# Optimization experiments

Hardware: AMD Instinct MI355X
Metric: run time of the kernel (lower is better)

## Reference

```python
import jax, jax.numpy as jnp
import numpy as np

B, P, N = 32, 128, 1000
EMB, H, QKV, FFH = 128, 8, 16, 128
LS = [11, 21]  # local_size + 1 per policy
PEN = -100000.0
CLIP = 10.0
EPS = 1e-5


def _policy_params(key, ls):
    ks = jax.random.split(key, 8)
    s = 0.05
    return dict(
        w1=jax.random.normal(ks[0], (2 * ls + 2, FFH)) * s, b1=jnp.zeros((FFH,)),
        w2=jax.random.normal(ks[1], (FFH, 2 * FFH)) * s, b2=jnp.zeros((2 * FFH,)),
        w3=jax.random.normal(ks[2], (2 * FFH, FFH)) * s, b3=jnp.zeros((FFH,)),
        w4=jax.random.normal(ks[3], (FFH, ls)) * 0.01, b4=jnp.zeros((ls,)),
        gamma=jnp.ones((2 * FFH,)), beta=jnp.zeros((2 * FFH,)),
    )


def setup_inputs() -> dict:
    key = jax.random.key(0)
    ks = jax.random.split(key, 16)
    s = 0.05
    d = {
        "encoded_last_node": jax.random.normal(ks[0], (B, P, EMB)),
        "load": jax.random.uniform(ks[1], (B, P)),
        "cur_dist": jax.random.uniform(ks[2], (B, P, N)),
        "cur_theta": jax.random.normal(ks[3], (B, P, N)),
        "ins_feat0": jax.random.normal(ks[4], (B, P, 1)),
        "ins_feat1": jax.random.normal(ks[5], (B, P, 1)),
        "ninf_mask": jnp.zeros((B, P, N)),
        "encoded_nodes": jax.random.normal(ks[6], (B, N, EMB)),
        "Wq_last": jax.random.normal(ks[7], (EMB + 1, H * QKV)) * s,
        "Wk": jax.random.normal(ks[8], (EMB, H * QKV)) * s,
        "Wv": jax.random.normal(ks[9], (EMB, H * QKV)) * s,
        "Wcomb": jax.random.normal(ks[10], (H * QKV, EMB)) * s,
        "bcomb": jnp.zeros((EMB,)),
    }
    for i, ls in enumerate(LS):
        pp = _policy_params(ks[11 + i], ls)
        for name, val in pp.items():
            d[f"p{i}_{name}"] = val
    return d


def _local_policy(theta, dist, f0, f1, w1, b1, w2, b2, w3, b3, w4, b4, gamma, beta, ls):
    # topk smallest distances
    neg_v, idx = jax.lax.top_k(-dist, ls)          # [B,P,ls]
    sd = -neg_v
    sd = sd / sd.max(-1, keepdims=True)
    st = jnp.take_along_axis(theta, idx, axis=-1)
    x = jnp.concatenate([sd, st, f0, f1], axis=-1)  # [B,P,2*ls+2]
    e = jax.nn.relu(x @ w1 + b1)
    h = jax.nn.relu(e @ w2 + b2)                    # [B,P,2*FFH]
    # InstanceNorm1d over the P (length) axis, per (batch, channel)
    mu = h.mean(axis=1, keepdims=True)
    var = h.var(axis=1, keepdims=True)
    h = (h - mu) * jax.lax.rsqrt(var + EPS) * gamma + beta
    e = jax.nn.relu(h @ w3 + b3)
    out = e @ w4 + b4 - sd                          # [B,P,ls]
    bi = jnp.arange(dist.shape[0])[:, None, None]
    pi = jnp.arange(dist.shape[1])[None, :, None]
    return jnp.full(dist.shape, PEN, dist.dtype).at[bi, pi, idx].set(out)


def reference(encoded_last_node, load, cur_dist, cur_theta, ins_feat0, ins_feat1,
              ninf_mask, encoded_nodes,
              Wq_last, Wk, Wv, Wcomb, bcomb,
              p0_w1, p0_b1, p0_w2, p0_b2, p0_w3, p0_b3, p0_w4, p0_b4, p0_gamma, p0_beta,
              p1_w1, p1_b1, p1_w2, p1_b2, p1_w3, p1_b3, p1_w4, p1_b4, p1_gamma, p1_beta):
    def rh(x):  # reshape_by_heads -> [B, H, n, QKV]
        b, n, _ = x.shape
        return x.reshape(b, n, H, QKV).transpose(0, 2, 1, 3)

    k = rh(encoded_nodes @ Wk)
    v = rh(encoded_nodes @ Wv)
    q = rh(jnp.concatenate([encoded_last_node, load[:, :, None]], axis=-1) @ Wq_last)

    score = jnp.einsum('bhpd,bhnd->bhpn', q, k) / jnp.sqrt(jnp.float32(QKV))
    score = score + ninf_mask[:, None, :, :]
    w = jax.nn.softmax(score, axis=-1)
    oc = jnp.einsum('bhpn,bhnd->bhpd', w, v).transpose(0, 2, 1, 3).reshape(B, P, H * QKV)
    mh = oc @ Wcomb + bcomb                                    # [B,P,EMB]

    sc = jnp.einsum('bpe,bne->bpn', mh, encoded_nodes) / jnp.sqrt(jnp.float32(EMB))

    sl0 = _local_policy(cur_theta, cur_dist, ins_feat0, ins_feat1,
                        p0_w1, p0_b1, p0_w2, p0_b2, p0_w3, p0_b3, p0_w4, p0_b4,
                        p0_gamma, p0_beta, LS[0])
    sl1 = _local_policy(cur_theta, cur_dist, ins_feat0, ins_feat1,
                        p1_w1, p1_b1, p1_w2, p1_b2, p1_w3, p1_b3, p1_w4, p1_b4,
                        p1_gamma, p1_beta, LS[1])
    sc = sc + (sl0 + sl1) / 2.0

    probs = jax.nn.softmax(CLIP * jnp.tanh(sc) + ninf_mask, axis=-1)
    return probs
```

## Files before the change

### kernel.cpp

```cpp
#include <hip/hip_runtime.h>
#include <math.h>

#define BB 32
#define PP 128
#define NN 1000
#define EMB 128
#define HH 8
#define FFH 128
#define PEN -100000.0f
#define CLIP 10.0f
#define EPS 1e-5f

__global__ __launch_bounds__(512) void mega1(
    const float* __restrict__ enc, const float* __restrict__ Wk, const float* __restrict__ Wv,
    float* __restrict__ Kb, float* __restrict__ Vb,
    const float* __restrict__ eln, const float* __restrict__ load,
    const float* __restrict__ Wq, float* __restrict__ Q,
    const float* __restrict__ mask, float* __restrict__ maskT,
    const float* __restrict__ dist, const float* __restrict__ theta,
    const float* __restrict__ f0, const float* __restrict__ f1,
    float* __restrict__ XS0, float* __restrict__ XS1,
    float* __restrict__ SD0, float* __restrict__ SD1, int* __restrict__ IDX) {
    __shared__ float smem[2112];
    int blk = blockIdx.x;
    int tid = threadIdx.x;
    if (blk < 512) {
        int half = blk & 1, chunk = (blk >> 1) & 7, b = blk >> 4;
        const float* W = half ? Wv : Wk;
        float* Ob = half ? Vb : Kb;
        int n0 = chunk * 125;
        float* A_s = smem;
        float* B_s = smem + 1056;
        int tr = tid >> 5, tc = tid & 31;
        float acc[8][4];
#pragma unroll
        for (int i = 0; i < 8; i++)
#pragma unroll
            for (int j = 0; j < 4; j++) acc[i][j] = 0.f;
        for (int kk = 0; kk < 128; kk += 8) {
#pragma unroll
            for (int f = tid; f < 1024; f += 512) {
                int node = f >> 3, k = f & 7;
                A_s[k * 132 + node] = (node < 125)
                    ? enc[((size_t)(b * 1000) + n0 + node) * 128 + kk + k] : 0.f;
            }
#pragma unroll
            for (int f = tid; f < 1024; f += 512) {
                int k = f >> 7, c = f & 127;
                B_s[k * 132 + c] = W[(kk + k) * 128 + c];
            }
            __syncthreads();
#pragma unroll
            for (int k = 0; k < 8; ++k) {
                float av[8], bv[4];
                *(float4*)&av[0] = *(const float4*)&A_s[k * 132 + tr * 8];
                *(float4*)&av[4] = *(const float4*)&A_s[k * 132 + tr * 8 + 4];
                *(float4*)&bv[0] = *(const float4*)&B_s[k * 132 + tc * 4];
#pragma unroll
                for (int i = 0; i < 8; ++i)
#pragma unroll
                    for (int j = 0; j < 4; ++j) acc[i][j] = fmaf(av[i], bv[j], acc[i][j]);
            }
            __syncthreads();
        }
#pragma unroll
        for (int i = 0; i < 8; ++i) {
            int node = tr * 8 + i;
            if (node < 125) {
                float4 o = {acc[i][0], acc[i][1], acc[i][2], acc[i][3]};
                *(float4*)(Ob + ((size_t)(b * 1000) + n0 + node) * 128 + tc * 4) = o;
            }
        }
    } else if (blk < 1024) {
        int r0 = (blk - 512) * 8;
        float* x_s = smem;
#pragma unroll
        for (int f = tid; f < 1024; f += 512) {
            int r = f >> 7, c = f & 127;
            x_s[r * 129 + c] = eln[(size_t)(r0 + r) * 128 + c];
        }
        if (tid < 8) x_s[tid * 129 + 128] = load[r0 + tid];
        __syncthreads();
        int rr = tid >> 7, c = tid & 127;
        float a0 = 0.f, a1 = 0.f;
#pragma unroll 4
        for (int k = 0; k < 128; ++k) {
            float wv = Wq[k * 128 + c];
            a0 = fmaf(x_s[rr * 129 + k], wv, a0);
            a1 = fmaf(x_s[(rr + 4) * 129 + k], wv, a1);
        }
        {
            float wv = Wq[16384 + c];
            a0 = fmaf(x_s[rr * 129 + 128], wv, a0);
            a1 = fmaf(x_s[(rr + 4) * 129 + 128], wv, a1);
        }
        Q[(size_t)(r0 + rr) * 128 + c] = a0 * 0.25f;
        Q[(size_t)(r0 + rr + 4) * 128 + c] = a1 * 0.25f;
    } else if (blk < 3072) {
        int t2 = (blk - 1024) * 2 + (tid >> 8);
        int tl = tid & 255;
        int b = t2 >> 7, pt = (t2 >> 5) & 3, nt = t2 & 31;
        int tx = tl & 31, ty = tl >> 5;
        float* t = smem + (tid >> 8) * 1056;
        int p0 = pt * 32, n0 = nt * 32;
#pragma unroll
        for (int r = 0; r < 32; r += 8) {
            int pp = p0 + ty + r, nn = n0 + tx;
            t[(ty + r) * 33 + tx] = (nn < 1000) ? mask[((size_t)b * 128 + pp) * 1000 + nn] : 0.f;
        }
        __syncthreads();
#pragma unroll
        for (int r = 0; r < 32; r += 8) {
            int nn = n0 + ty + r, pp = p0 + tx;
            if (nn < 1000) maskT[((size_t)b * 1000 + nn) * 128 + pp] = t[tx * 33 + ty + r];
        }
    } else {
        int w = tid >> 6, lane = tid & 63;
        int bp = (blk - 3072) * 8 + w;
        const float* drow = dist + (size_t)bp * 1000;
        unsigned long long key[16];
#pragma unroll
        for (int j = 0; j < 16; ++j) {
            int n = j * 64 + lane;
            key[j] = (n < 1000)
                ? ((((unsigned long long)__float_as_uint(drow[n])) << 32) | (unsigned)n)
                : ~0ull;
        }
        float myv = 0.f, v10 = 0.f, v20 = 0.f;
        int myi = 0;
        for (int t = 0; t < 21; ++t) {
            unsigned long long kmin = key[0];
            int jm = 0;
#pragma unroll
            for (int j = 1; j < 16; ++j)
                if (key[j] < kmin) { kmin = key[j]; jm = j; }
            unsigned long long g = kmin;
#pragma unroll
            for (int o = 1; o < 64; o <<= 1) {
                unsigned long long o2 = __shfl_xor(g, o, 64);
                g = (o2 < g) ? o2 : g;
            }
            if (kmin == g) key[jm] = ~0ull;
            float gv = __uint_as_float((unsigned)(g >> 32));
            if (t == lane) { myv = gv; myi = (int)(g & 0xffffffffu); }
            if (t == 10) v10 = gv;
            if (t == 20) v20 = gv;
        }
        if (lane < 21) {
            float th = theta[(size_t)bp * 1000 + myi];
            IDX[(size_t)bp * 21 + lane] = myi;
            float sd1 = myv / v20;
            XS1[(size_t)bp * 44 + lane] = sd1;
            XS1[(size_t)bp * 44 + 21 + lane] = th;
            SD1[(size_t)bp * 21 + lane] = sd1;
            if (lane < 11) {
                float sd0 = myv / v10;
                XS0[(size_t)bp * 24 + lane] = sd0;
                XS0[(size_t)bp * 24 + 11 + lane] = th;
                SD0[(size_t)bp * 11 + lane] = sd0;
            }
        }
        if (lane == 0) {
            float a = f0[bp], c = f1[bp];
            XS0[(size_t)bp * 24 + 22] = a;
            XS0[(size_t)bp * 24 + 23] = c;
            XS1[(size_t)bp * 44 + 42] = a;
            XS1[(size_t)bp * 44 + 43] = c;
        }
    }
}

__global__ __launch_bounds__(512) void attn5(const float* __restrict__ Q,
                                             const float* __restrict__ Kb,
                                             const float* __restrict__ Vb,
                                             const float* __restrict__ maskT,
                                             float* __restrict__ OC) {
    int blk = blockIdx.x;
    int b = blk & 31, h = blk >> 5;
    int tid = threadIdx.x;
    __shared__ float lds[32000];
    float4* K4 = (float4*)lds;
    float4* V4 = (float4*)(lds + 16000);
    const size_t baseKV = (size_t)b * 128000 + h * 16;
    for (int f = tid; f < 4000; f += 512) {
        int n = f >> 2, d4 = f & 3;
        K4[f] = *(const float4*)(Kb + baseKV + (size_t)n * 128 + d4 * 4);
        V4[f] = *(const float4*)(Vb + baseKV + (size_t)n * 128 + d4 * 4);
    }
    int pg = tid & 31, ng = tid >> 5;
    int p0 = pg * 4;
    float4 qr[4][4];
#pragma unroll
    for (int j = 0; j < 4; ++j) {
        const float* qp = Q + ((size_t)(b * 128 + p0 + j)) * 128 + h * 16;
#pragma unroll
        for (int d4 = 0; d4 < 4; ++d4) qr[j][d4] = *(const float4*)(qp + d4 * 4);
    }
    const float* mT = maskT + (size_t)b * 128000 + p0;
    __syncthreads();

    float4 z = {0.f, 0.f, 0.f, 0.f};
    float4 Oa[4][4];
    float l4[4] = {0.f, 0.f, 0.f, 0.f};
#pragma unroll
    for (int j = 0; j < 4; ++j)
#pragma unroll
        for (int d4 = 0; d4 < 4; ++d4) Oa[j][d4] = z;

    int nlim = (ng < 8) ? 63 : 62;
    int n = ng;
    float4 k0 = K4[n * 4], k1 = K4[n * 4 + 1], k2 = K4[n * 4 + 2], k3 = K4[n * 4 + 3];
    float4 v0 = V4[n * 4], v1 = V4[n * 4 + 1], v2 = V4[n * 4 + 2], v3 = V4[n * 4 + 3];
    float4 mv = *(const float4*)(mT + (size_t)n * 128);
#pragma unroll 1
    for (int i = 0; i < nlim; ++i) {
        int nn = n + 16;
        nn = (nn < 1000) ? nn : n;
        int nn4 = nn * 4;
        float4 K0 = K4[nn4], K1 = K4[nn4 + 1], K2 = K4[nn4 + 2], K3 = K4[nn4 + 3];
        float4 V0 = V4[nn4], V1 = V4[nn4 + 1], V2 = V4[nn4 + 2], V3 = V4[nn4 + 3];
        float4 MV = *(const float4*)(mT + (size_t)nn * 128);
        float mva[4] = {mv.x, mv.y, mv.z, mv.w};
#pragma unroll
        for (int j = 0; j < 4; ++j) {
            float sA = qr[j][0].x * k0.x;
            sA = fmaf(qr[j][0].y, k0.y, sA);
            sA = fmaf(qr[j][0].z, k0.z, sA);
            sA = fmaf(qr[j][0].w, k0.w, sA);
            sA = fmaf(qr[j][1].x, k1.x, sA);
            sA = fmaf(qr[j][1].y, k1.y, sA);
            sA = fmaf(qr[j][1].z, k1.z, sA);
            sA = fmaf(qr[j][1].w, k1.w, sA);
            float sB = fmaf(qr[j][2].x, k2.x, mva[j]);
            sB = fmaf(qr[j][2].y, k2.y, sB);
            sB = fmaf(qr[j][2].z, k2.z, sB);
            sB = fmaf(qr[j][2].w, k2.w, sB);
            sB = fmaf(qr[j][3].x, k3.x, sB);
            sB = fmaf(qr[j][3].y, k3.y, sB);
            sB = fmaf(qr[j][3].z, k3.z, sB);
            sB = fmaf(qr[j][3].w, k3.w, sB);
            float e = __expf(sA + sB);
            l4[j] += e;
            Oa[j][0].x = fmaf(e, v0.x, Oa[j][0].x);
            Oa[j][0].y = fmaf(e, v0.y, Oa[j][0].y);
            Oa[j][0].z = fmaf(e, v0.z, Oa[j][0].z);
            Oa[j][0].w = fmaf(e, v0.w, Oa[j][0].w);
            Oa[j][1].x = fmaf(e, v1.x, Oa[j][1].x);
            Oa[j][1].y = fmaf(e, v1.y, Oa[j][1].y);
            Oa[j][1].z = fmaf(e, v1.z, Oa[j][1].z);
            Oa[j][1].w = fmaf(e, v1.w, Oa[j][1].w);
            Oa[j][2].x = fmaf(e, v2.x, Oa[j][2].x);
            Oa[j][2].y = fmaf(e, v2.y, Oa[j][2].y);
            Oa[j][2].z = fmaf(e, v2.z, Oa[j][2].z);
            Oa[j][2].w = fmaf(e, v2.w, Oa[j][2].w);
            Oa[j][3].x = fmaf(e, v3.x, Oa[j][3].x);
            Oa[j][3].y = fmaf(e, v3.y, Oa[j][3].y);
            Oa[j][3].z = fmaf(e, v3.z, Oa[j][3].z);
            Oa[j][3].w = fmaf(e, v3.w, Oa[j][3].w);
        }
        k0 = K0; k1 = K1; k2 = K2; k3 = K3;
        v0 = V0; v1 = V1; v2 = V2; v3 = V3;
        mv = MV;
        n = nn;
    }
#pragma unroll
    for (int j = 0; j < 4; ++j) {
        l4[j] += __shfl_xor(l4[j], 32, 64);
#pragma unroll
        for (int d4 = 0; d4 < 4; ++d4) {
            Oa[j][d4].x += __shfl_xor(Oa[j][d4].x, 32, 64);
            Oa[j][d4].y += __shfl_xor(Oa[j][d4].y, 32, 64);
            Oa[j][d4].z += __shfl_xor(Oa[j][d4].z, 32, 64);
            Oa[j][d4].w += __shfl_xor(Oa[j][d4].w, 32, 64);
        }
    }
    __syncthreads();
    float* part = lds;
    if ((tid & 32) == 0) {
        int w = tid >> 6;
#pragma unroll
        for (int j = 0; j < 4; ++j) {
            float* pr = part + w * 2560 + (p0 + j) * 20;
#pragma unroll
            for (int d4 = 0; d4 < 4; ++d4) *(float4*)(pr + d4 * 4) = Oa[j][d4];
            pr[16] = l4[j];
        }
    }
    __syncthreads();
    {
        int p = tid >> 2, dg = tid & 3;
        float lsum = 0.f;
        float4 o = z;
#pragma unroll
        for (int w = 0; w < 8; ++w) {
            const float* pr = part + w * 2560 + p * 20;
            lsum += pr[16];
            float4 t = *(const float4*)(pr + dg * 4);
            o.x += t.x; o.y += t.y; o.z += t.z; o.w += t.w;
        }
        float inv = 1.f / lsum;
        float4 r = {o.x * inv, o.y * inv, o.z * inv, o.w * inv};
        *(float4*)(OC + ((size_t)(b * 128 + p)) * 128 + h * 16 + dg * 4) = r;
    }
}

__global__ __launch_bounds__(512) void pfront(
    const float* __restrict__ XS0, const float* __restrict__ XS1,
    const float* __restrict__ w1_0, const float* __restrict__ b1_0,
    const float* __restrict__ w2_0, const float* __restrict__ b2_0,
    const float* __restrict__ w1_1, const float* __restrict__ b1_1,
    const float* __restrict__ w2_1, const float* __restrict__ b2_1,
    float* __restrict__ Hb0, float* __restrict__ Hb1) {
    __shared__ float smem[12320];
    int fb = blockIdx.x;
    int tid = threadIdx.x;
    int pol = fb & 1, colT = (fb >> 1) & 1, rowT = fb >> 2;
    int r0 = rowT * 64, c0 = colT * 128;
    const float* XS = pol ? XS1 : XS0;
    const float* w1 = pol ? w1_1 : w1_0;
    const float* b1 = pol ? b1_1 : b1_0;
    const float* w2 = pol ? w2_1 : w2_0;
    const float* b2 = pol ? b2_1 : b2_0;
    float* Hb = pol ? Hb1 : Hb0;
    int XSW = pol ? 44 : 24;
    float* xs_s = smem;
    float* e_s = smem + 2816;
    float* B_s = smem + 11264;
    for (int f = tid; f < 64 * XSW; f += 512) {
        int r = f / XSW, k = f % XSW;
        xs_s[r * 44 + k] = XS[(size_t)(r0 + r) * XSW + k];
    }
    __syncthreads();
#pragma unroll
    for (int i = 0; i < 16; ++i) {
        int f = tid + i * 512;
        int r = f >> 7, c = f & 127;
        float acc = b1[c];
        for (int k = 0; k < XSW; ++k) acc = fmaf(xs_s[r * 44 + k], w1[k * 128 + c], acc);
        e_s[r * 132 + c] = fmaxf(acc, 0.f);
    }
    __syncthreads();
    int tr = tid >> 5, tc = tid & 31;
    float acc[4][4];
#pragma unroll
    for (int jj = 0; jj < 4; ++jj) {
        float bb = b2[c0 + tc * 4 + jj];
#pragma unroll
        for (int j = 0; j < 4; ++j) acc[j][jj] = bb;
    }
    for (int kk = 0; kk < 128; kk += 8) {
#pragma unroll
        for (int f = tid; f < 1024; f += 512) {
            int k = f >> 7, c = f & 127;
            B_s[k * 132 + c] = w2[(size_t)(kk + k) * 256 + c0 + c];
        }
        __syncthreads();
#pragma unroll
        for (int k = 0; k < 8; ++k) {
            float av[4], bv[4];
#pragma unroll
            for (int j = 0; j < 4; ++j) av[j] = e_s[(tr * 4 + j) * 132 + kk + k];
            *(float4*)&bv[0] = *(const float4*)&B_s[k * 132 + tc * 4];
#pragma unroll
            for (int j = 0; j < 4; ++j)
#pragma unroll
                for (int jj = 0; jj < 4; ++jj) acc[j][jj] = fmaf(av[j], bv[jj], acc[j][jj]);
        }
        __syncthreads();
    }
#pragma unroll
    for (int j = 0; j < 4; ++j) {
        float4 o = {fmaxf(acc[j][0], 0.f), fmaxf(acc[j][1], 0.f),
                    fmaxf(acc[j][2], 0.f), fmaxf(acc[j][3], 0.f)};
        *(float4*)(Hb + (size_t)(r0 + tr * 4 + j) * 256 + c0 + tc * 4) = o;
    }
}

__global__ __launch_bounds__(512) void mega3(
    const float* __restrict__ OC, const float* __restrict__ Wc, const float* __restrict__ bc,
    float* __restrict__ MH,
    const float* __restrict__ Hb0, const float* __restrict__ Hb1,
    float* __restrict__ MUb, float* __restrict__ RSb) {
    __shared__ float smem[1056];
    int blk = blockIdx.x;
    int tid = threadIdx.x;
    if (blk < 512) {
        int r0 = blk * 8;
        float* x_s = smem;
#pragma unroll
        for (int f = tid; f < 1024; f += 512) {
            int r = f >> 7, c = f & 127;
            x_s[r * 129 + c] = OC[(size_t)(r0 + r) * 128 + c];
        }
        __syncthreads();
        int rr = tid >> 7, c = tid & 127;
        float a0 = bc[c], a1 = a0;
#pragma unroll 4
        for (int k = 0; k < 128; ++k) {
            float wv = Wc[k * 128 + c];
            a0 = fmaf(x_s[rr * 129 + k], wv, a0);
            a1 = fmaf(x_s[(rr + 4) * 129 + k], wv, a1);
        }
        MH[(size_t)(r0 + rr) * 128 + c] = a0;
        MH[(size_t)(r0 + rr + 4) * 128 + c] = a1;
    } else {
        int ib = blk - 512;
        int pol = ib & 1, b = ib >> 1;
        const float* Hb = pol ? Hb1 : Hb0;
        int c = tid & 255, half = tid >> 8;
        float s = 0.f, s2 = 0.f;
        int pbase = half * 64;
        for (int p = pbase; p < pbase + 64; ++p) {
            float v = Hb[((size_t)(b * 128 + p)) * 256 + c];
            s += v;
            s2 += v * v;
        }
        float* s_s = smem;
        float* s2_s = smem + 512;
        s_s[half * 256 + c] = s;
        s2_s[half * 256 + c] = s2;
        __syncthreads();
        if (half == 0) {
            float S = s_s[c] + s_s[256 + c];
            float S2 = s2_s[c] + s2_s[256 + c];
            float mu = S * (1.f / 128.f);
            float var = S2 * (1.f / 128.f) - mu * mu;
            MUb[pol * 8192 + b * 256 + c] = mu;
            RSb[pol * 8192 + b * 256 + c] = rsqrtf(var + EPS);
        }
    }
}

__global__ __launch_bounds__(512) void mega4(
    const float* __restrict__ MH, const float* __restrict__ enc, float* __restrict__ SC,
    const float* __restrict__ Hb0, const float* __restrict__ Hb1,
    const float* __restrict__ MUb, const float* __restrict__ RSb,
    const float* __restrict__ g0, const float* __restrict__ be0,
    const float* __restrict__ w3_0, const float* __restrict__ b3_0,
    const float* __restrict__ w4_0, const float* __restrict__ b4_0,
    const float* __restrict__ g1, const float* __restrict__ be1,
    const float* __restrict__ w3_1, const float* __restrict__ b3_1,
    const float* __restrict__ w4_1, const float* __restrict__ b4_1,
    const float* __restrict__ SD0, const float* __restrict__ SD1,
    float* __restrict__ OUT0, float* __restrict__ OUT1) {
    __shared__ float smem[12160];
    int blk = blockIdx.x;
    int tid = threadIdx.x;
    if (blk < 512) {
        int ph = blk & 1, chunk = (blk >> 1) & 7, b = blk >> 4;
        int n0 = chunk * 125, p0 = ph * 64;
        float* A_s = smem;
        float* B_s = smem + 544;
        int tr = tid >> 5, tc = tid & 31;
        float acc[4][4];
#pragma unroll
        for (int i = 0; i < 4; i++)
#pragma unroll
            for (int j = 0; j < 4; j++) acc[i][j] = 0.f;
        for (int kk = 0; kk < 128; kk += 8) {
            {
                int r = tid >> 3, k = tid & 7;
                A_s[k * 68 + r] = MH[((size_t)(b * 128) + p0 + r) * 128 + kk + k];
            }
#pragma unroll
            for (int f = tid; f < 1024; f += 512) {
                int nn = f >> 3, k = f & 7;
                B_s[k * 132 + nn] = (nn < 125)
                    ? enc[((size_t)(b * 1000) + n0 + nn) * 128 + kk + k] : 0.f;
            }
            __syncthreads();
#pragma unroll
            for (int k = 0; k < 8; ++k) {
                float av[4], bv[4];
                *(float4*)&av[0] = *(const float4*)&A_s[k * 68 + tr * 4];
                *(float4*)&bv[0] = *(const float4*)&B_s[k * 132 + tc * 4];
#pragma unroll
                for (int i = 0; i < 4; ++i)
#pragma unroll
                    for (int j = 0; j < 4; ++j) acc[i][j] = fmaf(av[i], bv[j], acc[i][j]);
            }
            __syncthreads();
        }
        const float invs = 0.08838834764831845f;
#pragma unroll
        for (int i = 0; i < 4; ++i) {
            int pp = p0 + tr * 4 + i;
#pragma unroll
            for (int j = 0; j < 4; ++j) {
                int n = tc * 4 + j;
                if (n < 125) SC[((size_t)(b * 128) + pp) * 1000 + n0 + n] = acc[i][j] * invs;
            }
        }
    } else {
        int bb2 = blk - 512;
        int pol = bb2 & 1, rowT = bb2 >> 1;
        int r0 = rowT * 64, b = r0 >> 7;
        const float* Hb = pol ? Hb1 : Hb0;
        const float* MU = MUb + pol * 8192 + b * 256;
        const float* RS = RSb + pol * 8192 + b * 256;
        const float* gg = pol ? g1 : g0;
        const float* bbv = pol ? be1 : be0;
        const float* w3 = pol ? w3_1 : w3_0;
        const float* pb3 = pol ? b3_1 : b3_0;
        const float* w4 = pol ? w4_1 : w4_0;
        const float* pb4 = pol ? b4_1 : b4_0;
        const float* SD = pol ? SD1 : SD0;
        float* OUT = pol ? OUT1 : OUT0;
        int ls = pol ? 21 : 11;
        float* scale_s = smem;
        float* shift_s = smem + 256;
        float* A_s = smem + 512;
        float* B_s = smem + 1600;
        float* e2_s = smem + 3712;
        if (tid < 256) {
            float sc = RS[tid] * gg[tid];
            scale_s[tid] = sc;
            shift_s[tid] = bbv[tid] - MU[tid] * sc;
        }
        __syncthreads();
        int tr = tid >> 5, tc = tid & 31;
        float acc[4][4];
#pragma unroll
        for (int jj = 0; jj < 4; ++jj) {
            float bv = pb3[tc * 4 + jj];
#pragma unroll
            for (int j = 0; j < 4; ++j) acc[j][jj] = bv;
        }
        for (int kk = 0; kk < 256; kk += 16) {
#pragma unroll
            for (int f = tid; f < 1024; f += 512) {
                int r = f >> 4, k = f & 15;
                float v = Hb[(size_t)(r0 + r) * 256 + kk + k];
                A_s[k * 68 + r] = v * scale_s[kk + k] + shift_s[kk + k];
            }
#pragma unroll
            for (int f = tid; f < 2048; f += 512) {
                int k = f >> 7, c = f & 127;
                B_s[k * 132 + c] = w3[(size_t)(kk + k) * 128 + c];
            }
            __syncthreads();
#pragma unroll
            for (int k = 0; k < 16; ++k) {
                float av[4], bv[4];
                *(float4*)&av[0] = *(const float4*)&A_s[k * 68 + tr * 4];
                *(float4*)&bv[0] = *(const float4*)&B_s[k * 132 + tc * 4];
#pragma unroll
                for (int j = 0; j < 4; ++j)
#pragma unroll
                    for (int jj = 0; jj < 4; ++jj) acc[j][jj] = fmaf(av[j], bv[jj], acc[j][jj]);
            }
            __syncthreads();
        }
#pragma unroll
        for (int j = 0; j < 4; ++j) {
            float4 o = {fmaxf(acc[j][0], 0.f), fmaxf(acc[j][1], 0.f),
                        fmaxf(acc[j][2], 0.f), fmaxf(acc[j][3], 0.f)};
            *(float4*)&e2_s[(tr * 4 + j) * 132 + tc * 4] = o;
        }
        __syncthreads();
        for (int o = tid; o < 64 * ls; o += 512) {
            int row = o / ls, c = o % ls;
            float a = pb4[c];
#pragma unroll 4
            for (int k = 0; k < 128; ++k) a = fmaf(e2_s[row * 132 + k], w4[k * ls + c], a);
            OUT[(size_t)(r0 + row) * ls + c] = a - SD[(size_t)(r0 + row) * ls + c];
        }
    }
}

__device__ inline float blockReduceMaxF(float v, volatile float* red) {
#pragma unroll
    for (int o = 32; o > 0; o >>= 1) v = fmaxf(v, __shfl_xor(v, o, 64));
    if ((threadIdx.x & 63) == 0) red[threadIdx.x >> 6] = v;
    __syncthreads();
    float r = fmaxf(fmaxf(red[0], red[1]), fmaxf(red[2], red[3]));
    __syncthreads();
    return r;
}

__device__ inline float blockReduceSumF(float v, volatile float* red) {
#pragma unroll
    for (int o = 32; o > 0; o >>= 1) v += __shfl_xor(v, o, 64);
    if ((threadIdx.x & 63) == 0) red[threadIdx.x >> 6] = v;
    __syncthreads();
    float r = red[0] + red[1] + red[2] + red[3];
    __syncthreads();
    return r;
}

__global__ void final_softmax(const float* SC, const float* __restrict__ mask,
                              const int* __restrict__ IDX, const float* __restrict__ OUT0,
                              const float* __restrict__ OUT1, float* out) {
    int bp = blockIdx.x;
    int tid = threadIdx.x;
    __shared__ float a0[1000];
    __shared__ float a1[1000];
    __shared__ float red[4];
    for (int n = tid; n < 1000; n += 256) {
        a0[n] = PEN;
        a1[n] = PEN;
    }
    __syncthreads();
    if (tid < 11) a0[IDX[bp * 21 + tid]] = OUT0[bp * 11 + tid];
    if (tid < 21) a1[IDX[bp * 21 + tid]] = OUT1[bp * 21 + tid];
    __syncthreads();
    float logit[4];
    float lmax = -INFINITY;
    {
        int i = 0;
        for (int n = tid; n < 1000; n += 256, i++) {
            float sc = SC[(size_t)bp * 1000 + n] + 0.5f * (a0[n] + a1[n]);
            float zz = __expf(2.f * sc);
            float t = 1.f - 2.f / (zz + 1.f);
            float lg = CLIP * t + mask[(size_t)bp * 1000 + n];
            logit[i] = lg;
            lmax = fmaxf(lmax, lg);
        }
    }
    float m = blockReduceMaxF(lmax, red);
    float lsum = 0.f;
    {
        int i = 0;
        for (int n = tid; n < 1000; n += 256, i++) {
            float e = __expf(logit[i] - m);
            logit[i] = e;
            lsum += e;
        }
    }
    float s = blockReduceSumF(lsum, red);
    float inv = 1.f / s;
    {
        int i = 0;
        for (int n = tid; n < 1000; n += 256, i++) out[(size_t)bp * 1000 + n] = logit[i] * inv;
    }
}

extern "C" void kernel_launch(void* const* d_in, const int* in_sizes, int n_in,
                              void* d_out, int out_size, void* d_ws, size_t ws_size,
                              hipStream_t stream) {
    const float* eln   = (const float*)d_in[0];
    const float* load  = (const float*)d_in[1];
    const float* dist  = (const float*)d_in[2];
    const float* theta = (const float*)d_in[3];
    const float* f0    = (const float*)d_in[4];
    const float* f1    = (const float*)d_in[5];
    const float* mask  = (const float*)d_in[6];
    const float* enc   = (const float*)d_in[7];
    const float* Wq    = (const float*)d_in[8];
    const float* Wk    = (const float*)d_in[9];
    const float* Wv    = (const float*)d_in[10];
    const float* Wc    = (const float*)d_in[11];
    const float* bc    = (const float*)d_in[12];
    const float* p0w1 = (const float*)d_in[13];
    const float* p0b1 = (const float*)d_in[14];
    const float* p0w2 = (const float*)d_in[15];
    const float* p0b2 = (const float*)d_in[16];
    const float* p0w3 = (const float*)d_in[17];
    const float* p0b3 = (const float*)d_in[18];
    const float* p0w4 = (const float*)d_in[19];
    const float* p0b4 = (const float*)d_in[20];
    const float* p0g  = (const float*)d_in[21];
    const float* p0be = (const float*)d_in[22];
    const float* p1w1 = (const float*)d_in[23];
    const float* p1b1 = (const float*)d_in[24];
    const float* p1w2 = (const float*)d_in[25];
    const float* p1b2 = (const float*)d_in[26];
    const float* p1w3 = (const float*)d_in[27];
    const float* p1b3 = (const float*)d_in[28];
    const float* p1w4 = (const float*)d_in[29];
    const float* p1b4 = (const float*)d_in[30];
    const float* p1g  = (const float*)d_in[31];
    const float* p1be = (const float*)d_in[32];

    float* out = (float*)d_out;

    float* ws = (float*)d_ws;
    float* Kb   = ws;
    float* Vb   = Kb + 4096000;
    float* Qb   = Vb + 4096000;
    float* OCb  = Qb + 524288;
    float* MHb  = OCb + 524288;
    float* Hb0  = MHb + 524288;
    float* Hb1  = Hb0 + 1048576;
    float* MUb  = Hb1 + 1048576;
    float* RSb  = MUb + 16384;
    float* SD0  = RSb + 16384;
    float* SD1  = SD0 + 45056;
    float* OUT0 = SD1 + 86016;
    float* OUT1 = OUT0 + 45056;
    int*   IDX  = (int*)(OUT1 + 86016);
    float* XS0  = (float*)(IDX + 86016);
    float* XS1  = XS0 + 98304;

    float* maskT = out;
    float* SC = out;

    mega1<<<3584, 512, 0, stream>>>(enc, Wk, Wv, Kb, Vb,
                                    eln, load, Wq, Qb,
                                    mask, maskT,
                                    dist, theta, f0, f1, XS0, XS1, SD0, SD1, IDX);
    attn5<<<256, 512, 0, stream>>>(Qb, Kb, Vb, maskT, OCb);
    pfront<<<256, 512, 0, stream>>>(XS0, XS1,
                                    p0w1, p0b1, p0w2, p0b2,
                                    p1w1, p1b1, p1w2, p1b2,
                                    Hb0, Hb1);
    mega3<<<576, 512, 0, stream>>>(OCb, Wc, bc, MHb, Hb0, Hb1, MUb, RSb);
    mega4<<<640, 512, 0, stream>>>(MHb, enc, SC,
                                   Hb0, Hb1, MUb, RSb,
                                   p0g, p0be, p0w3, p0b3, p0w4, p0b4,
                                   p1g, p1be, p1w3, p1b3, p1w4, p1b4,
                                   SD0, SD1, OUT0, OUT1);
    final_softmax<<<BB * PP, 256, 0, stream>>>(SC, mask, IDX, OUT0, OUT1, out);
}
```

Before: 255.2 us.

## Load K/V GEMM tiles in two wide passes and tile the Q projection

The K/V projection path now stages 64 of the k dimension at once with float4 global loads, using two passes instead of sixteen 8-wide steps. This cuts the number of barriers and makes the global loads wider. The Q projection is rewritten from a per-row dot-product loop into a register-tiled shared-memory GEMM over 64 rows per block, shrinking its block count from 512 to 64 and shifting the later branch indices to match. Static shared memory grows to about 65KB for every block in the fused launch, including the mask-transpose and top-k blocks, which can lower occupancy across the whole kernel.

```diff
diff --git a/kernel.cpp b/kernel.cpp
--- a/kernel.cpp
+++ b/kernel.cpp
@@ -21,7 +21,7 @@
     const float* __restrict__ f0, const float* __restrict__ f1,
     float* __restrict__ XS0, float* __restrict__ XS1,
     float* __restrict__ SD0, float* __restrict__ SD1, int* __restrict__ IDX) {
-    __shared__ float smem[2112];
+    __shared__ float smem[16640];
     int blk = blockIdx.x;
     int tid = threadIdx.x;
     if (blk < 512) {
@@ -30,38 +30,44 @@
         float* Ob = half ? Vb : Kb;
         int n0 = chunk * 125;
         float* A_s = smem;
-        float* B_s = smem + 1056;
+        float* B_s = smem + 8192;
         int tr = tid >> 5, tc = tid & 31;
         float acc[8][4];
 #pragma unroll
         for (int i = 0; i < 8; i++)
 #pragma unroll
             for (int j = 0; j < 4; j++) acc[i][j] = 0.f;
-        for (int kk = 0; kk < 128; kk += 8) {
-#pragma unroll
-            for (int f = tid; f < 1024; f += 512) {
-                int node = f >> 3, k = f & 7;
-                A_s[k * 132 + node] = (node < 125)
-                    ? enc[((size_t)(b * 1000) + n0 + node) * 128 + kk + k] : 0.f;
-            }
-#pragma unroll
-            for (int f = tid; f < 1024; f += 512) {
-                int k = f >> 7, c = f & 127;
-                B_s[k * 132 + c] = W[(kk + k) * 128 + c];
+        for (int pass = 0; pass < 2; ++pass) {
+            if (pass) __syncthreads();
+            for (int f = tid; f < 2000; f += 512) {
+                int node = f >> 4, k4 = (f & 15) * 4;
+                float4 v = *(const float4*)(enc + ((size_t)(b * 1000) + n0 + node) * 128
+                                            + pass * 64 + k4);
+                A_s[(k4 + 0) * 128 + node] = v.x;
+                A_s[(k4 + 1) * 128 + node] = v.y;
+                A_s[(k4 + 2) * 128 + node] = v.z;
+                A_s[(k4 + 3) * 128 + node] = v.w;
+            }
+            for (int f = tid; f < 2048; f += 512) {
+                int k = f >> 5, c4 = (f & 31) * 4;
+                float4 v = *(const float4*)(W + (size_t)(pass * 64 + k) * 128 + c4);
+                B_s[k * 132 + c4 + 0] = v.x;
+                B_s[k * 132 + c4 + 1] = v.y;
+                B_s[k * 132 + c4 + 2] = v.z;
+                B_s[k * 132 + c4 + 3] = v.w;
             }
             __syncthreads();
-#pragma unroll
-            for (int k = 0; k < 8; ++k) {
+#pragma unroll 8
+            for (int k = 0; k < 64; ++k) {
                 float av[8], bv[4];
-                *(float4*)&av[0] = *(const float4*)&A_s[k * 132 + tr * 8];
-                *(float4*)&av[4] = *(const float4*)&A_s[k * 132 + tr * 8 + 4];
+                *(float4*)&av[0] = *(const float4*)&A_s[k * 128 + tr * 8];
+                *(float4*)&av[4] = *(const float4*)&A_s[k * 128 + tr * 8 + 4];
                 *(float4*)&bv[0] = *(const float4*)&B_s[k * 132 + tc * 4];
 #pragma unroll
                 for (int i = 0; i < 8; ++i)
 #pragma unroll
                     for (int j = 0; j < 4; ++j) acc[i][j] = fmaf(av[i], bv[j], acc[i][j]);
             }
-            __syncthreads();
         }
 #pragma unroll
         for (int i = 0; i < 8; ++i) {
@@ -71,33 +77,60 @@
                 *(float4*)(Ob + ((size_t)(b * 1000) + n0 + node) * 128 + tc * 4) = o;
             }
         }
-    } else if (blk < 1024) {
-        int r0 = (blk - 512) * 8;
-        float* x_s = smem;
-#pragma unroll
-        for (int f = tid; f < 1024; f += 512) {
-            int r = f >> 7, c = f & 127;
-            x_s[r * 129 + c] = eln[(size_t)(r0 + r) * 128 + c];
-        }
-        if (tid < 8) x_s[tid * 129 + 128] = load[r0 + tid];
-        __syncthreads();
-        int rr = tid >> 7, c = tid & 127;
-        float a0 = 0.f, a1 = 0.f;
-#pragma unroll 4
-        for (int k = 0; k < 128; ++k) {
-            float wv = Wq[k * 128 + c];
-            a0 = fmaf(x_s[rr * 129 + k], wv, a0);
-            a1 = fmaf(x_s[(rr + 4) * 129 + k], wv, a1);
-        }
-        {
-            float wv = Wq[16384 + c];
-            a0 = fmaf(x_s[rr * 129 + 128], wv, a0);
-            a1 = fmaf(x_s[(rr + 4) * 129 + 128], wv, a1);
-        }
-        Q[(size_t)(r0 + rr) * 128 + c] = a0 * 0.25f;
-        Q[(size_t)(r0 + rr + 4) * 128 + c] = a1 * 0.25f;
-    } else if (blk < 3072) {
-        int t2 = (blk - 1024) * 2 + (tid >> 8);
+    } else if (blk < 576) {
+        int r0 = (blk - 512) * 64;
+        float* A_s = smem;
+        float* B_s = smem + 8192;
+        int tr = tid >> 5, tc = tid & 31;
+        float acc[4][4];
+#pragma unroll
+        for (int i = 0; i < 4; i++)
+#pragma unroll
+            for (int j = 0; j < 4; j++) acc[i][j] = 0.f;
+        for (int pass = 0; pass < 2; ++pass) {
+            if (pass) __syncthreads();
+            for (int f = tid; f < 1024; f += 512) {
+                int row = f >> 4, k4 = (f & 15) * 4;
+                float4 v = *(const float4*)(eln + (size_t)(r0 + row) * 128 + pass * 64 + k4);
+                A_s[(k4 + 0) * 128 + row] = v.x;
+                A_s[(k4 + 1) * 128 + row] = v.y;
+                A_s[(k4 + 2) * 128 + row] = v.z;
+                A_s[(k4 + 3) * 128 + row] = v.w;
+            }
+            for (int f = tid; f < 2048; f += 512) {
+                int k = f >> 5, c4 = (f & 31) * 4;
+                float4 v = *(const float4*)(Wq + (size_t)(pass * 64 + k) * 128 + c4);
+                B_s[k * 132 + c4 + 0] = v.x;
+                B_s[k * 132 + c4 + 1] = v.y;
+                B_s[k * 132 + c4 + 2] = v.z;
+                B_s[k * 132 + c4 + 3] = v.w;
+            }
+            __syncthreads();
+#pragma unroll 8
+            for (int k = 0; k < 64; ++k) {
+                float av[4], bv[4];
+                *(float4*)&av[0] = *(const float4*)&A_s[k * 128 + tr * 4];
+                *(float4*)&bv[0] = *(const float4*)&B_s[k * 132 + tc * 4];
+#pragma unroll
+                for (int i = 0; i < 4; ++i)
+#pragma unroll
+                    for (int j = 0; j < 4; ++j) acc[i][j] = fmaf(av[i], bv[j], acc[i][j]);
+            }
+        }
+#pragma unroll
+        for (int i = 0; i < 4; ++i) {
+            int row = r0 + tr * 4 + i;
+            float lv = load[row];
+#pragma unroll
+            for (int j = 0; j < 4; ++j) {
+                float wv = Wq[16384 + tc * 4 + j];
+                acc[i][j] = fmaf(lv, wv, acc[i][j]) * 0.25f;
+            }
+            float4 o = {acc[i][0], acc[i][1], acc[i][2], acc[i][3]};
+            *(float4*)(Q + (size_t)row * 128 + tc * 4) = o;
+        }
+    } else if (blk < 2624) {
+        int t2 = (blk - 576) * 2 + (tid >> 8);
         int tl = tid & 255;
         int b = t2 >> 7, pt = (t2 >> 5) & 3, nt = t2 & 31;
         int tx = tl & 31, ty = tl >> 5;
@@ -116,7 +149,7 @@
         }
     } else {
         int w = tid >> 6, lane = tid & 63;
-        int bp = (blk - 3072) * 8 + w;
+        int bp = (blk - 2624) * 8 + w;
         const float* drow = dist + (size_t)bp * 1000;
         unsigned long long key[16];
 #pragma unroll
@@ -695,7 +728,7 @@
     float* maskT = out;
     float* SC = out;
 
-    mega1<<<3584, 512, 0, stream>>>(enc, Wk, Wv, Kb, Vb,
+    mega1<<<3136, 512, 0, stream>>>(enc, Wk, Wv, Kb, Vb,
                                     eln, load, Wq, Qb,
                                     mask, maskT,
                                     dist, theta, f0, f1, XS0, XS1, SD0, SD1, IDX);
```

After: 251.2 us. Within noise of the previous version (-1.6%).
